# Optimization experiments

Hardware: AMD Instinct MI355X
Metric: run time of the kernel (lower is better)

The kernel has to match this reference:

```python
import jax, jax.numpy as jnp
import numpy as np

# Dimensions
NT, NS = 1000, 2048   # timesteps, basins
NF, NG = 6, 32        # forcing channels, static attributes
NH, NR, HS = 16, 8, 256  # buckets, routing taps, hidden size
NK, NGD = 3, 9        # len(kDict)=3 (km,ki,ke), len(gDict)=9


def setup_inputs() -> dict:
    key = jax.random.key(0)
    ks = jax.random.split(key, 16)
    # Physically plausible forcings: Prcp/Evp nonnegative, T1<=T2 (min/max temp)
    Prcp = jax.random.uniform(ks[0], (NT, NS)) * 10.0
    Evp = jax.random.uniform(ks[1], (NT, NS)) * 5.0
    Tm = jax.random.normal(ks[2], (NT, NS)) * 10.0
    T1 = Tm - jax.random.uniform(ks[3], (NT, NS)) * 5.0
    T2 = Tm + jax.random.uniform(ks[4], (NT, NS)) * 5.0
    Rad = jax.random.uniform(ks[5], (NT, NS))
    Hum = jax.random.uniform(ks[6], (NT, NS))
    x = jnp.stack([Prcp, Evp, T1, T2, Rad, Hum], axis=-1)  # [nt, ns, 6]
    xc = jax.random.normal(ks[7], (NS, NG))

    def lin(k, fan_in, fan_out, s=0.05):
        k1, k2 = jax.random.split(k)
        return (jax.random.normal(k1, (fan_in, fan_out)) * s,
                jax.random.normal(k2, (fan_out,)) * s)

    W_fc, b_fc = lin(ks[8], NG, HS)
    W_r, b_r = lin(ks[9], HS, NH * (NR + 1))
    W_g, b_g = lin(ks[10], HS, NH * NGD)
    W_kin, b_kin = lin(ks[11], 4, HS)
    W_kout, b_kout = lin(ks[12], HS, NH * NK)
    return dict(x=x, xc=xc, W_fc=W_fc, b_fc=b_fc, W_r=W_r, b_r=b_r,
                W_g=W_g, b_g=b_g, W_kin=W_kin, b_kin=b_kin,
                W_kout=W_kout, b_kout=b_kout)


def _hardsigmoid(v):
    return jnp.clip(v / 6.0 + 0.5, 0.0, 1.0)


def _forward(x, xc, W_fc, b_fc, W_r, b_r, W_g, b_g, W_kin, b_kin, W_kout, b_kout):
    nt, ns, _ = x.shape
    Prcp, Evp, T1, T2 = x[..., 0], x[..., 1], x[..., 2], x[..., 3]
    f = x[..., 2:]                        # [nt, ns, 4] (T1,T2,Rad,Hum)

    # ---- getParam (eval mode: DropMask is identity) ----
    state = xc @ W_fc + b_fc              # [ns, hs]
    pK = jnp.tanh(f @ W_kin + b_kin + state) @ W_kout + b_kout  # [nt, ns, nh*3]
    hG = jnp.tanh(state)
    pG = hG @ W_g + b_g                   # [ns, nh*9]
    pR = hG @ W_r + b_r                   # [ns, nh*(nr+1)]

    # sepParam(K): km=exp, ki=relu, ke=exp  -> time-varying [nt, ns, nh]
    km = jnp.exp(pK[..., 0 * NH:1 * NH])
    ki = jax.nn.relu(pK[..., 1 * NH:2 * NH])
    ke = jnp.exp(pK[..., 2 * NH:3 * NH])

    # sepParam(G): static [ns, nh]
    g = lambda i: pG[..., i * NH:(i + 1) * NH]
    kp = jax.nn.sigmoid(g(0))
    ks_ = jax.nn.sigmoid(g(1))
    kd = jax.nn.sigmoid(g(2))
    gd = jax.nn.sigmoid(g(3))
    gl = (jax.nn.sigmoid(g(4)) * 10.0) ** 3
    qb = jax.nn.relu(g(5)) / 10.0
    ga = jax.nn.softmax(g(6), axis=-1)    # area weights over buckets
    gi = _hardsigmoid(g(7)) / 2.0
    ge = jax.nn.relu(g(8))

    # onePeakWeight: unimodal routing weights [ns, nh, nr]
    r = pR.reshape(ns, NH, NR + 1)
    s = jax.nn.softmax(r, axis=-1)
    c = jnp.cumsum(s, axis=-1)
    w = jnp.minimum(c, 1.0 - c + s)[..., :NR]
    wr = w / jnp.sum(w, axis=-1, keepdims=True)

    # divideP: snow/liquid split from min/max temperature crossing 0 C
    fl = jnp.clip(T2 / (T2 - T1 + 1e-5), 0.0, 1.0)  # liquid fraction
    Pl = (Prcp * fl)[..., None]           # [nt, ns, 1]
    Ps = (Prcp * (1.0 - fl))[..., None]
    Ev = Evp[..., None]

    # ---- bucket.step recurrence over time (the custom-scan hot loop) ----
    def step(carry, inp):
        Sf, Ss, Sg = carry                # each [ns, nh]
        Ps_t, Pl_t, Ev_t, km_t, ki_t, ke_t = inp
        # snow bucket: accumulate, melt capped by degree-day factor km
        Sf = Sf + Ps_t
        qf = jnp.minimum(Sf, km_t)
        Sf = Sf - qf
        # partition inflow: impervious/direct fraction gi
        inflow = qf + Pl_t
        qd = inflow * gi
        Ss = Ss + inflow * (1.0 - gi)
        # evapotranspiration
        E = jnp.minimum(jnp.maximum(Ss, 0.0), Ev_t * ke_t * ge)
        Ss = Ss - E
        # interflow capped by ki
        qi = jnp.minimum(ki_t, jnp.maximum(Ss, 0.0))
        Ss = Ss - qi
        # quick flow above capacity gl, slow drainage below
        qp = kp * jnp.maximum(Ss - gl, 0.0)
        qsa = ks_ * jnp.clip(Ss, 0.0, gl)
        Ss = Ss - qp - qsa
        # deep/groundwater bucket: fraction gd percolates, linear reservoir kd + baseflow qb
        Sg = Sg + qsa * gd
        qg = kd * Sg + qb
        Sg = Sg * (1.0 - kd)
        q = qp + qsa * (1.0 - gd) + qg + qd + qi
        return (Sf, Ss, Sg), q

    init = (jnp.zeros((ns, NH), x.dtype),
            jnp.zeros((ns, NH), x.dtype),
            jnp.zeros((ns, NH), x.dtype))
    _, Qp = jax.lax.scan(step, init, (Ps, Pl, Ev, km, ki, ke))  # [nt, ns, nh]

    # routing: valid temporal convolution with per-bucket unit hydrograph wr
    Tout = nt - NR + 1
    Q = jnp.zeros((Tout, ns, NH), Qp.dtype)
    for rr in range(NR):  # NR is a small fixed constant
        Q = Q + Qp[NR - 1 - rr: nt - rr] * wr[..., rr]
    yOut = jnp.sum(Q * ga, axis=-1)       # [Tout, ns]
    return yOut


def reference(x, xc, W_fc, b_fc, W_r, b_r, W_g, b_g, W_kin, b_kin, W_kout, b_kout):
    return _forward(x, xc, W_fc, b_fc, W_r, b_r, W_g, b_g, W_kin, b_kin, W_kout, b_kout)
```

## Files before the change

kernel.cpp:

```cpp
#include <hip/hip_runtime.h>
#include <hip/hip_bf16.h>

#define NT   1000
#define NS   2048
#define NH   16
#define NR   8
#define HS   256
#define TOUT 993

typedef __attribute__((ext_vector_type(8))) short short8;
typedef __attribute__((ext_vector_type(4))) float f32x4;

__device__ __forceinline__ ushort f2bf(float f) {
    union { float f; unsigned int u; } v; v.f = f;
    unsigned int u = v.u;
    return (ushort)((u + 0x7fffu + ((u >> 16) & 1u)) >> 16);
}
__device__ __forceinline__ float bf2f(ushort u) {
    union { unsigned int i; float f; } v; v.i = ((unsigned int)u) << 16; return v.f;
}
__device__ __forceinline__ unsigned int packbf2(float lo, float hi) {
    union { __hip_bfloat162 b; unsigned int u; } v;
    v.b = __float22bfloat162_rn(make_float2(lo, hi));
    return v.u;
}
__device__ __forceinline__ float sigf(float x) { return 1.f / (1.f + __expf(-x)); }
__device__ __forceinline__ float fast_tanh(float z) {
    float e = exp2f(z * 2.885390082f);
    return 1.f - 2.f * __builtin_amdgcn_rcpf(e + 1.f);
}
template<int CTRL>
__device__ __forceinline__ float dpp_add(float v) {
    int s = __builtin_amdgcn_update_dpp(0, __builtin_bit_cast(int, v), CTRL, 0xf, 0xf, true);
    return v + __builtin_bit_cast(float, s);
}
__device__ __forceinline__ void gll16(const void* g, void* l) {
    __builtin_amdgcn_global_load_lds((const __attribute__((address_space(1))) unsigned int*)g,
                                     (__attribute__((address_space(3))) unsigned int*)l, 16, 0, 0);
}
__device__ __forceinline__ void gll4(const void* g, void* l) {
    __builtin_amdgcn_global_load_lds((const __attribute__((address_space(1))) unsigned int*)g,
                                     (__attribute__((address_space(3))) unsigned int*)l, 4, 0, 0);
}

__global__ __launch_bounds__(256) void kA(
    const float* __restrict__ xc, const float* __restrict__ W_fc, const float* __restrict__ b_fc,
    const float* __restrict__ W_r, const float* __restrict__ b_r,
    const float* __restrict__ W_g, const float* __restrict__ b_g,
    const float* __restrict__ W_kin, const float* __restrict__ b_kin,
    const float* __restrict__ W_kout,
    float* __restrict__ stateK, float* __restrict__ params,
    ushort* __restrict__ Wt_g, ushort* __restrict__ whlo_g)
{
    __shared__ float xcs[32];
    __shared__ float hG[256];
    __shared__ float pGR[288];
    const int s = blockIdx.x, tid = threadIdx.x;

    if (tid < 32) xcs[tid] = xc[s * 32 + tid];
    __syncthreads();

    float acc = b_fc[tid];
#pragma unroll 8
    for (int k = 0; k < 32; ++k) acc = fmaf(xcs[k], W_fc[k * 256 + tid], acc);
    stateK[s * 256 + tid] = acc + b_kin[tid];
    hG[tid] = tanhf(acc);
    __syncthreads();

    for (int j = tid; j < 288; j += 256) {
        const float* W = (j < 144) ? W_g : W_r;
        const float* b = (j < 144) ? b_g : b_r;
        int col = (j < 144) ? j : (j - 144);
        float a = b[col];
#pragma unroll 4
        for (int k = 0; k < 256; ++k) a = fmaf(hG[k], W[k * 144 + col], a);
        pGR[j] = a;
    }
    __syncthreads();

    if (tid < 16) {
        const int h = tid;
        float g0 = pGR[h],       g1 = pGR[16 + h],  g2 = pGR[32 + h];
        float g3 = pGR[48 + h],  g4 = pGR[64 + h],  g5 = pGR[80 + h];
        float g6 = pGR[96 + h],  g7 = pGR[112 + h], g8 = pGR[128 + h];
        float kp = sigf(g0), ksg = sigf(g1), kd = sigf(g2), gd = sigf(g3);
        float t4 = sigf(g4) * 10.f; float gl = t4 * t4 * t4;
        float qb = fmaxf(g5, 0.f) * 0.1f;
        float gi = fminf(fmaxf(g7 * (1.f / 6.f) + 0.5f, 0.f), 1.f) * 0.5f;
        float ge = fmaxf(g8, 0.f);
        float m = g6;
        for (int o = 1; o < 16; o <<= 1) m = fmaxf(m, __shfl_xor(m, o));
        float e = __expf(g6 - m), esum = e;
        for (int o = 1; o < 16; o <<= 1) esum += __shfl_xor(esum, o);
        float ga = e / esum;
        float r[9], rm = -1e30f;
#pragma unroll
        for (int i = 0; i < 9; ++i) { r[i] = pGR[144 + h * 9 + i]; rm = fmaxf(rm, r[i]); }
        float er[9], es = 0.f;
#pragma unroll
        for (int i = 0; i < 9; ++i) { er[i] = __expf(r[i] - rm); es += er[i]; }
        float inv_es = 1.f / es, c = 0.f, wsum = 0.f, w[8];
#pragma unroll
        for (int i = 0; i < 8; ++i) {
            float si = er[i] * inv_es; c += si;
            float wi = fminf(c, 1.f - c + si);
            w[i] = wi; wsum += wi;
        }
        const int base = s * 16 + h;
        params[0 * 32768 + base] = kp;       params[1 * 32768 + base] = ksg;
        params[2 * 32768 + base] = kd;       params[3 * 32768 + base] = gd;
        params[4 * 32768 + base] = gl;       params[5 * 32768 + base] = qb;
        params[6 * 32768 + base] = gi;       params[7 * 32768 + base] = 1.f - gi;
        params[8 * 32768 + base] = 1.f - kd; params[9 * 32768 + base] = 1.f - gd;
        params[10 * 32768 + base] = ge;
        float sc = ga / wsum;
#pragma unroll
        for (int i = 0; i < 8; ++i) params[(11 + i) * 32768 + base] = w[i] * sc;
    }

    if (s == 0) {
        for (int i = tid; i < 48 * 256; i += 256) {
            int col = i % 48, slot = i / 48;
            int kk = slot >> 5, q = (slot >> 3) & 3, j = slot & 7;
            int h = kk * 32 + ((j < 4) ? (q * 4 + j) : (16 + q * 4 + (j - 4)));
            Wt_g[col * 264 + slot] = f2bf(W_kout[h * 48 + col]);
        }
        {
            const int h = tid;
#pragma unroll
            for (int f = 0; f < 4; ++f) {
                float w = W_kin[f * 256 + h];
                ushort hi = f2bf(w);
                float lo = w - bf2f(hi);
                whlo_g[h * 8 + f] = hi;
                whlo_g[h * 8 + 4 + f] = f2bf(lo);
            }
        }
    }
}

__global__ __launch_bounds__(256, 3) void kB(
    const float* __restrict__ x,
    const float* __restrict__ stateK, const float* __restrict__ b_kout,
    const ushort* __restrict__ Wt_g, const ushort* __restrict__ whlo_g,
    const float* __restrict__ params,
    unsigned int* __restrict__ kmki, ushort* __restrict__ kevA,
    float2* __restrict__ pspl)
{
    __shared__ ushort Wt[48 * 264];
    __shared__ float  stS[16 * 260];
    __shared__ ushort whloS[2048];
    __shared__ float  geS[256];
    __shared__ float  evS[4][5][16];
    const int tid = threadIdx.x;
    const int st = blockIdx.x & 127;
    const int tg = blockIdx.x >> 7;
    const int s0 = st << 4;

    for (int i = tid; i < 3168; i += 256)
        ((uint2*)Wt)[i] = ((const uint2*)Wt_g)[i];
#pragma unroll
    for (int i = tid; i < 1024; i += 256) {
        int row = i >> 6, c = (i & 63) << 2;
        *(float4*)(stS + row * 260 + c) = *(const float4*)(stateK + (s0 + row) * 256 + c);
    }
    *(float4*)(whloS + tid * 8) = ((const float4*)whlo_g)[tid];
    geS[tid] = params[10 * 32768 + s0 * 16 + tid];
    __syncthreads();

    const int wv = tid >> 6, lane = tid & 63;
    const int mi = lane & 15, quad = lane >> 4;
    const int site = s0 + mi;
    const int t0 = tg * 20 + wv * 5;

    float xf[5][4];
#pragma unroll
    for (int ti = 0; ti < 5; ++ti) {
        const int t = t0 + ti;
        const int xb = (t * 2048 + site) * 6;
        float2 u23 = *(const float2*)(x + xb + 2);
        float2 u45 = *(const float2*)(x + xb + 4);
        xf[ti][0] = u23.x; xf[ti][1] = u23.y; xf[ti][2] = u45.x; xf[ti][3] = u45.y;
        if (lane < 16) {
            float2 u01 = *(const float2*)(x + xb);
            float fl = fminf(fmaxf(u23.y * __builtin_amdgcn_rcpf(u23.y - u23.x + 1e-5f), 0.f), 1.f);
            const int sg = st * 4 + (mi >> 2), sl = mi & 3;
            pspl[(sg * 1000 + t) * 4 + sl] = make_float2(u01.x * (1.f - fl), u01.x * fl);
            evS[wv][ti][mi] = u01.y;
        }
    }

    unsigned int bfr[5][4];
#pragma unroll
    for (int ti = 0; ti < 5; ++ti) {
        const float x0 = xf[ti][0], x1 = xf[ti][1], x2 = xf[ti][2], x3 = xf[ti][3];
        unsigned int h01 = packbf2(x0, x1), h23 = packbf2(x2, x3);
        float l0 = x0 - bf2f((ushort)(h01 & 0xffffu));
        float l1 = x1 - bf2f((ushort)(h01 >> 16));
        float l2 = x2 - bf2f((ushort)(h23 & 0xffffu));
        float l3 = x3 - bf2f((ushort)(h23 >> 16));
        unsigned int l01 = packbf2(l0, l1), l23 = packbf2(l2, l3);
        bfr[ti][0] = (quad == 0) ? h01 : (quad == 1 ? l01 : 0u);
        bfr[ti][1] = (quad == 0) ? h23 : (quad == 1 ? l23 : 0u);
        bfr[ti][2] = (quad == 0) ? h01 : 0u;
        bfr[ti][3] = (quad == 0) ? h23 : 0u;
    }

    const float*  stp = stS + mi * 260;
    const ushort* Wt0 = Wt + mi * 264 + quad * 8;
    const int q4 = quad * 4;

    f32x4 acc[5][3];
#pragma unroll
    for (int ti = 0; ti < 5; ++ti)
#pragma unroll
        for (int j = 0; j < 3; ++j) acc[ti][j] = (f32x4){0.f, 0.f, 0.f, 0.f};

#pragma unroll 1
    for (int kk = 0; kk < 8; ++kk) {
        const int ko = kk * 32;
        union { short8 s; unsigned int u[4]; } W0, W1, A0, A1;
        W0.s = *(const short8*)(whloS + (ko + mi) * 8);
        W1.s = *(const short8*)(whloS + (ko + 16 + mi) * 8);
        A0.u[0] = (quad <= 1) ? W0.u[0] : 0u;
        A0.u[1] = (quad <= 1) ? W0.u[1] : 0u;
        A0.u[2] = (quad == 0) ? W0.u[2] : 0u;
        A0.u[3] = (quad == 0) ? W0.u[3] : 0u;
        A1.u[0] = (quad <= 1) ? W1.u[0] : 0u;
        A1.u[1] = (quad <= 1) ? W1.u[1] : 0u;
        A1.u[2] = (quad == 0) ? W1.u[2] : 0u;
        A1.u[3] = (quad == 0) ? W1.u[3] : 0u;
        f32x4 c0 = *(const f32x4*)(stp + ko + q4);
        f32x4 c1 = *(const f32x4*)(stp + ko + 16 + q4);
        short8 b0 = *(const short8*)(Wt0 + ko);
        short8 b1 = *(const short8*)(Wt0 + 16 * 264 + ko);
        short8 b2 = *(const short8*)(Wt0 + 32 * 264 + ko);
#pragma unroll
        for (int ti = 0; ti < 5; ++ti) {
            union { short8 s; unsigned int u[4]; } B;
            B.u[0] = bfr[ti][0]; B.u[1] = bfr[ti][1];
            B.u[2] = bfr[ti][2]; B.u[3] = bfr[ti][3];
            f32x4 z0 = __builtin_amdgcn_mfma_f32_16x16x32_bf16(A0.s, B.s, c0, 0, 0, 0);
            f32x4 z1 = __builtin_amdgcn_mfma_f32_16x16x32_bf16(A1.s, B.s, c1, 0, 0, 0);
            union { short8 s; unsigned int u[4]; } a;
            a.u[0] = packbf2(fast_tanh(z0[0]), fast_tanh(z0[1]));
            a.u[1] = packbf2(fast_tanh(z0[2]), fast_tanh(z0[3]));
            a.u[2] = packbf2(fast_tanh(z1[0]), fast_tanh(z1[1]));
            a.u[3] = packbf2(fast_tanh(z1[2]), fast_tanh(z1[3]));
            acc[ti][0] = __builtin_amdgcn_mfma_f32_16x16x32_bf16(a.s, b0, acc[ti][0], 0, 0, 0);
            acc[ti][1] = __builtin_amdgcn_mfma_f32_16x16x32_bf16(a.s, b1, acc[ti][1], 0, 0, 0);
            acc[ti][2] = __builtin_amdgcn_mfma_f32_16x16x32_bf16(a.s, b2, acc[ti][2], 0, 0, 0);
        }
    }

    const float bo0 = b_kout[mi], bo1 = b_kout[16 + mi], bo2 = b_kout[32 + mi];
#pragma unroll
    for (int ti = 0; ti < 5; ++ti) {
        const int t = t0 + ti;
#pragma unroll
        for (int reg = 0; reg < 4; ++reg) {
            const int sl = quad * 4 + reg;
            float km = __expf(acc[ti][0][reg] + bo0);
            float ki = fmaxf(acc[ti][1][reg] + bo1, 0.f);
            float ke = __expf(acc[ti][2][reg] + bo2);
            float kev = ke * evS[wv][ti][sl] * geS[sl * 16 + mi];
            const int idx = ((s0 + sl) * 1000 + t) * 16 + mi;
            kmki[idx] = (unsigned int)f2bf(km) | ((unsigned int)f2bf(ki) << 16);
            kevA[idx] = f2bf(kev);
        }
    }
}

#define KM_STRIDE 4160
#define KE_BASE   16640
#define KE_STRIDE 2080
#define PS_BASE   24960
#define BUF_SZ    27008
__global__ __launch_bounds__(64, 1) void kC(
    const unsigned int* __restrict__ kmki, const ushort* __restrict__ kevA,
    const float2* __restrict__ pspl,
    const float* __restrict__ params, float* __restrict__ yOut)
{
    __shared__ char lds[2 * BUF_SZ];
    const int tid = threadIdx.x;
    const int sg = blockIdx.x;
    const int sl = tid >> 4;
    const int s = sg * 4 + sl;
    const int h = tid & 15;
    const int gid = s * 16 + h;

    const float kp  = params[0 * 32768 + gid];
    const float ks_ = params[1 * 32768 + gid];
    const float kd  = params[2 * 32768 + gid];
    const float gd  = params[3 * 32768 + gid];
    const float gl  = params[4 * 32768 + gid];
    const float qbv = params[5 * 32768 + gid];
    const float gi  = params[6 * 32768 + gid];
    const float gi1 = params[7 * 32768 + gid];
    const float kd1 = params[8 * 32768 + gid];
    const float gd1 = params[9 * 32768 + gid];
    float wrga[8];
#pragma unroll
    for (int i = 0; i < 8; ++i) wrga[i] = params[(11 + i) * 32768 + gid];

    float Sf = 0.f, Ss = 0.f, Sg = 0.f;
    float qh[8];
#pragma unroll
    for (int i = 0; i < 8; ++i) qh[i] = 0.f;

    const char* kmG = (const char*)kmki;
    const char* keG = (const char*)kevA;
    const char* psG = (const char*)pspl;

#define STAGE(c, TAIL) do {                                                     \
        char* L = lds + ((c) & 1) * BUF_SZ;                                     \
        _Pragma("unroll")                                                       \
        for (int q = 0; q < 4; ++q) {                                           \
            const char* gk = kmG + ((size_t)(sg * 4 + q) * 1000 + (c) * 64) * 64; \
            const char* ge = keG + ((size_t)(sg * 4 + q) * 1000 + (c) * 64) * 32; \
            char* lk = L + q * KM_STRIDE;                                       \
            char* le = L + KE_BASE + q * KE_STRIDE;                             \
            if (!(TAIL)) {                                                      \
                _Pragma("unroll")                                               \
                for (int k = 0; k < 4; ++k) gll16(gk + k * 1024 + tid * 16, lk + k * 1024); \
                _Pragma("unroll")                                               \
                for (int k = 0; k < 2; ++k) gll16(ge + k * 1024 + tid * 16, le + k * 1024); \
            } else {                                                            \
                _Pragma("unroll")                                               \
                for (int k = 0; k < 2; ++k) gll16(gk + k * 1024 + tid * 16, lk + k * 1024); \
                _Pragma("unroll")                                               \
                for (int k = 0; k < 2; ++k) gll4(gk + 2048 + k * 256 + tid * 4, lk + 2048 + k * 256); \
                gll16(ge + tid * 16, le);                                       \
                gll4(ge + 1024 + tid * 4, le + 1024);                           \
            }                                                                   \
        }                                                                       \
        const char* gp = psG + ((size_t)sg * 1000 + (c) * 64) * 32;             \
        char* lp = L + PS_BASE;                                                 \
        if (!(TAIL)) { gll16(gp + tid * 16, lp); gll16(gp + 1024 + tid * 16, lp + 1024); } \
        else         { gll16(gp + tid * 16, lp); gll4(gp + 1024 + tid * 4, lp + 1024); }   \
    } while (0)

#define COMPUTE(c, NSB) do {                                                    \
        const char* L = lds + ((c) & 1) * BUF_SZ;                               \
        const char* lk = L + sl * KM_STRIDE + h * 4;                            \
        const char* le = L + KE_BASE + sl * KE_STRIDE + h * 2;                  \
        const char* lp = L + PS_BASE + sl * 8;                                  \
        for (int sb = 0; sb < (NSB); ++sb) {                                    \
            unsigned int a[8]; ushort e[8]; float2 p[8];                        \
            _Pragma("unroll")                                                   \
            for (int i = 0; i < 8; ++i) {                                       \
                const int tt = sb * 8 + i;                                      \
                a[i] = *(const unsigned int*)(lk + tt * 64);                    \
                e[i] = *(const ushort*)(le + tt * 32);                          \
                p[i] = *(const float2*)(lp + tt * 32);                          \
            }                                                                   \
            float z[8];                                                         \
            _Pragma("unroll")                                                   \
            for (int i = 0; i < 8; ++i) {                                       \
                float km = __builtin_bit_cast(float, a[i] << 16);               \
                float ki = __builtin_bit_cast(float, a[i] & 0xffff0000u);       \
                float kev = __builtin_bit_cast(float, ((unsigned int)e[i]) << 16); \
                float ps = p[i].x, pl = p[i].y;                                 \
                Sf += ps;                                                       \
                float qf = fminf(Sf, km); Sf -= qf;                             \
                float inflow = qf + pl;                                         \
                float qd = inflow * gi;                                         \
                Ss = fmaf(inflow, gi1, Ss);                                     \
                float E = fminf(Ss, kev); Ss -= E;                              \
                float qi = fminf(ki, Ss); Ss -= qi;                             \
                float qp = kp * fmaxf(Ss - gl, 0.f);                            \
                float qsa = ks_ * fminf(Ss, gl);                                \
                Ss -= qp + qsa;                                                 \
                Sg = fmaf(qsa, gd, Sg);                                         \
                float qg = fmaf(kd, Sg, qbv);                                   \
                Sg *= kd1;                                                      \
                float q = fmaf(qsa, gd1, qp) + qg + qd + qi;                    \
                qh[i] = q;                                                      \
                float v = 0.f;                                                  \
                _Pragma("unroll")                                               \
                for (int k = 0; k < 8; ++k) v = fmaf(wrga[k], qh[(i - k) & 7], v); \
                z[i] = v;                                                       \
            }                                                                   \
            _Pragma("unroll")                                                   \
            for (int i = 0; i < 8; ++i) z[i] = dpp_add<0xB1>(z[i]);             \
            _Pragma("unroll")                                                   \
            for (int i = 0; i < 8; ++i) z[i] = dpp_add<0x4E>(z[i]);             \
            _Pragma("unroll")                                                   \
            for (int i = 0; i < 8; ++i) z[i] = dpp_add<0x141>(z[i]);            \
            _Pragma("unroll")                                                   \
            for (int i = 0; i < 8; ++i) z[i] = dpp_add<0x140>(z[i]);            \
            if (h == 0) {                                                       \
                _Pragma("unroll")                                               \
                for (int i = 0; i < 8; ++i) {                                   \
                    const int t = (c) * 64 + sb * 8 + i;                        \
                    if (t >= 7) yOut[(t - 7) * 2048 + s] = z[i];                \
                }                                                               \
            }                                                                   \
        }                                                                       \
    } while (0)

    STAGE(0, false);
    for (int c = 0; c < 16; ++c) {
        if (c < 15) {
            if (c + 1 == 15) STAGE(15, true);
            else             STAGE(c + 1, false);
            asm volatile("s_waitcnt vmcnt(26)" ::: "memory");
        } else {
            asm volatile("s_waitcnt vmcnt(0)" ::: "memory");
        }
        if (c == 15) COMPUTE(15, 5);
        else         COMPUTE(c, 8);
        asm volatile("" ::: "memory");
    }
#undef STAGE
#undef COMPUTE
}

extern "C" void kernel_launch(void* const* d_in, const int* in_sizes, int n_in,
                              void* d_out, int out_size, void* d_ws, size_t ws_size,
                              hipStream_t stream) {
    const float* x      = (const float*)d_in[0];
    const float* xc     = (const float*)d_in[1];
    const float* W_fc   = (const float*)d_in[2];
    const float* b_fc   = (const float*)d_in[3];
    const float* W_r    = (const float*)d_in[4];
    const float* b_r    = (const float*)d_in[5];
    const float* W_g    = (const float*)d_in[6];
    const float* b_g    = (const float*)d_in[7];
    const float* W_kin  = (const float*)d_in[8];
    const float* b_kin  = (const float*)d_in[9];
    const float* W_kout = (const float*)d_in[10];
    const float* b_kout = (const float*)d_in[11];
    float* yOut = (float*)d_out;

    char* ws = (char*)d_ws;
    float*  stateK = (float*)(ws + 0);
    float*  params = (float*)(ws + (2 << 20));
    ushort* Wt_g   = (ushort*)(ws + (6 << 20));
    ushort* whlo_g = (ushort*)(ws + (6 << 20) + (64 << 10));
    char*   p      = ws + (6 << 20) + (128 << 10);
    float2* pspl   = (float2*)p;
    unsigned int* kmki = (unsigned int*)(p + 16384000);
    ushort* kevA   = (ushort*)(p + 16384000 + 131072000);

    hipLaunchKernelGGL(kA, dim3(2048), dim3(256), 0, stream,
                       xc, W_fc, b_fc, W_r, b_r, W_g, b_g, W_kin, b_kin, W_kout,
                       stateK, params, Wt_g, whlo_g);
    hipLaunchKernelGGL(kB, dim3(128 * 50), dim3(256), 0, stream,
                       x, stateK, b_kout, Wt_g, whlo_g, params, kmki, kevA, pspl);
    hipLaunchKernelGGL(kC, dim3(512), dim3(64), 0, stream,
                       kmki, kevA, pspl, params, yOut);
}
```

Measured before the change: 528.3 us.

## Software-pipeline routing convolution one block behind the bucket scan

Splits the per-8-step block into a scan phase and a convolution/reduce/store phase. The convolution for the previous block runs after the current block's scan, so the serial scan dependency chain can interleave with independent FMA, DPP and store work. The convolution also uses two partial accumulators to shorten its own chain. This costs extra registers for the two history arrays, adds a trailing flush call, and forces the loops not to unroll.

```diff
diff --git a/kernel.cpp b/kernel.cpp
--- a/kernel.cpp
+++ b/kernel.cpp
@@ -304,9 +304,9 @@
     for (int i = 0; i < 8; ++i) wrga[i] = params[(11 + i) * 32768 + gid];
 
     float Sf = 0.f, Ss = 0.f, Sg = 0.f;
-    float qh[8];
-#pragma unroll
-    for (int i = 0; i < 8; ++i) qh[i] = 0.f;
+    float qcur[8], qp1[8], qp2[8];
+#pragma unroll
+    for (int i = 0; i < 8; ++i) { qcur[i] = 0.f; qp1[i] = 0.f; qp2[i] = 0.f; }
 
     const char* kmG = (const char*)kmki;
     const char* keG = (const char*)kevA;
@@ -340,66 +340,75 @@
         else         { gll16(gp + tid * 16, lp); gll4(gp + 1024 + tid * 4, lp + 1024); }   \
     } while (0)
 
-#define COMPUTE(c, NSB) do {                                                    \
+#define SCANB(c, sb) do {                                                       \
         const char* L = lds + ((c) & 1) * BUF_SZ;                               \
-        const char* lk = L + sl * KM_STRIDE + h * 4;                            \
-        const char* le = L + KE_BASE + sl * KE_STRIDE + h * 2;                  \
-        const char* lp = L + PS_BASE + sl * 8;                                  \
-        for (int sb = 0; sb < (NSB); ++sb) {                                    \
-            unsigned int a[8]; ushort e[8]; float2 p[8];                        \
+        const char* lk = L + sl * KM_STRIDE + h * 4 + (sb) * 512;               \
+        const char* le = L + KE_BASE + sl * KE_STRIDE + h * 2 + (sb) * 256;     \
+        const char* lp = L + PS_BASE + sl * 8 + (sb) * 256;                     \
+        unsigned int a[8]; ushort e[8]; float2 p[8];                            \
+        _Pragma("unroll")                                                       \
+        for (int i = 0; i < 8; ++i) {                                           \
+            a[i] = *(const unsigned int*)(lk + i * 64);                         \
+            e[i] = *(const ushort*)(le + i * 32);                               \
+            p[i] = *(const float2*)(lp + i * 32);                               \
+        }                                                                       \
+        _Pragma("unroll")                                                       \
+        for (int i = 0; i < 8; ++i) {                                           \
+            float km = __builtin_bit_cast(float, a[i] << 16);                   \
+            float ki = __builtin_bit_cast(float, a[i] & 0xffff0000u);           \
+            float kev = __builtin_bit_cast(float, ((unsigned int)e[i]) << 16);  \
+            float ps = p[i].x, pl = p[i].y;                                     \
+            Sf += ps;                                                           \
+            float qf = fminf(Sf, km); Sf -= qf;                                 \
+            float inflow = qf + pl;                                             \
+            float qd = inflow * gi;                                             \
+            Ss = fmaf(inflow, gi1, Ss);                                         \
+            float E = fminf(Ss, kev); Ss -= E;                                  \
+            float qi = fminf(ki, Ss); Ss -= qi;                                 \
+            float qp = kp * fmaxf(Ss - gl, 0.f);                                \
+            float qsa = ks_ * fminf(Ss, gl);                                    \
+            Ss -= qp + qsa;                                                     \
+            Sg = fmaf(qsa, gd, Sg);                                             \
+            float qg = fmaf(kd, Sg, qbv);                                       \
+            Sg *= kd1;                                                          \
+            qcur[i] = fmaf(qsa, gd1, qp) + qg + qd + qi;                        \
+        }                                                                       \
+    } while (0)
+
+#define CONV_STORE(m) do {                                                      \
+        float z[8];                                                             \
+        _Pragma("unroll")                                                       \
+        for (int i = 0; i < 8; ++i) {                                           \
+            float za = wrga[6] * ((i >= 6) ? qp1[i - 6] : qp2[i + 2]);          \
+            za = fmaf(wrga[4], (i >= 4) ? qp1[i - 4] : qp2[i + 4], za);         \
+            za = fmaf(wrga[2], (i >= 2) ? qp1[i - 2] : qp2[i + 6], za);         \
+            za = fmaf(wrga[0], qp1[i], za);                                     \
+            float zb = wrga[7] * ((i >= 7) ? qp1[i - 7] : qp2[i + 1]);          \
+            zb = fmaf(wrga[5], (i >= 5) ? qp1[i - 5] : qp2[i + 3], zb);         \
+            zb = fmaf(wrga[3], (i >= 3) ? qp1[i - 3] : qp2[i + 5], zb);         \
+            zb = fmaf(wrga[1], (i >= 1) ? qp1[i - 1] : qp2[i + 7], zb);         \
+            z[i] = za + zb;                                                     \
+        }                                                                       \
+        _Pragma("unroll")                                                       \
+        for (int i = 0; i < 8; ++i) z[i] = dpp_add<0xB1>(z[i]);                 \
+        _Pragma("unroll")                                                       \
+        for (int i = 0; i < 8; ++i) z[i] = dpp_add<0x4E>(z[i]);                 \
+        _Pragma("unroll")                                                       \
+        for (int i = 0; i < 8; ++i) z[i] = dpp_add<0x141>(z[i]);                \
+        _Pragma("unroll")                                                       \
+        for (int i = 0; i < 8; ++i) z[i] = dpp_add<0x140>(z[i]);                \
+        if (h == 0) {                                                           \
             _Pragma("unroll")                                                   \
             for (int i = 0; i < 8; ++i) {                                       \
-                const int tt = sb * 8 + i;                                      \
-                a[i] = *(const unsigned int*)(lk + tt * 64);                    \
-                e[i] = *(const ushort*)(le + tt * 32);                          \
-                p[i] = *(const float2*)(lp + tt * 32);                          \
-            }                                                                   \
-            float z[8];                                                         \
-            _Pragma("unroll")                                                   \
-            for (int i = 0; i < 8; ++i) {                                       \
-                float km = __builtin_bit_cast(float, a[i] << 16);               \
-                float ki = __builtin_bit_cast(float, a[i] & 0xffff0000u);       \
-                float kev = __builtin_bit_cast(float, ((unsigned int)e[i]) << 16); \
-                float ps = p[i].x, pl = p[i].y;                                 \
-                Sf += ps;                                                       \
-                float qf = fminf(Sf, km); Sf -= qf;                             \
-                float inflow = qf + pl;                                         \
-                float qd = inflow * gi;                                         \
-                Ss = fmaf(inflow, gi1, Ss);                                     \
-                float E = fminf(Ss, kev); Ss -= E;                              \
-                float qi = fminf(ki, Ss); Ss -= qi;                             \
-                float qp = kp * fmaxf(Ss - gl, 0.f);                            \
-                float qsa = ks_ * fminf(Ss, gl);                                \
-                Ss -= qp + qsa;                                                 \
-                Sg = fmaf(qsa, gd, Sg);                                         \
-                float qg = fmaf(kd, Sg, qbv);                                   \
-                Sg *= kd1;                                                      \
-                float q = fmaf(qsa, gd1, qp) + qg + qd + qi;                    \
-                qh[i] = q;                                                      \
-                float v = 0.f;                                                  \
-                _Pragma("unroll")                                               \
-                for (int k = 0; k < 8; ++k) v = fmaf(wrga[k], qh[(i - k) & 7], v); \
-                z[i] = v;                                                       \
-            }                                                                   \
-            _Pragma("unroll")                                                   \
-            for (int i = 0; i < 8; ++i) z[i] = dpp_add<0xB1>(z[i]);             \
-            _Pragma("unroll")                                                   \
-            for (int i = 0; i < 8; ++i) z[i] = dpp_add<0x4E>(z[i]);             \
-            _Pragma("unroll")                                                   \
-            for (int i = 0; i < 8; ++i) z[i] = dpp_add<0x141>(z[i]);            \
-            _Pragma("unroll")                                                   \
-            for (int i = 0; i < 8; ++i) z[i] = dpp_add<0x140>(z[i]);            \
-            if (h == 0) {                                                       \
-                _Pragma("unroll")                                               \
-                for (int i = 0; i < 8; ++i) {                                   \
-                    const int t = (c) * 64 + sb * 8 + i;                        \
-                    if (t >= 7) yOut[(t - 7) * 2048 + s] = z[i];                \
-                }                                                               \
+                const int t = (m) * 8 + i;                                      \
+                if (t >= 7) yOut[(t - 7) * 2048 + s] = z[i];                    \
             }                                                                   \
         }                                                                       \
     } while (0)
 
     STAGE(0, false);
+    int g = 0;
+#pragma unroll 1
     for (int c = 0; c < 16; ++c) {
         if (c < 15) {
             if (c + 1 == 15) STAGE(15, true);
@@ -408,12 +417,20 @@
         } else {
             asm volatile("s_waitcnt vmcnt(0)" ::: "memory");
         }
-        if (c == 15) COMPUTE(15, 5);
-        else         COMPUTE(c, 8);
+        const int NSB = (c == 15) ? 5 : 8;
+#pragma unroll 1
+        for (int sb = 0; sb < NSB; ++sb, ++g) {
+            SCANB(c, sb);
+            CONV_STORE(g - 1);
+#pragma unroll
+            for (int i = 0; i < 8; ++i) { qp2[i] = qp1[i]; qp1[i] = qcur[i]; }
+        }
         asm volatile("" ::: "memory");
     }
+    CONV_STORE(124);
 #undef STAGE
-#undef COMPUTE
+#undef SCANB
+#undef CONV_STORE
 }
 
 extern "C" void kernel_launch(void* const* d_in, const int* in_sizes, int n_in,
```

After: 519.3 us. No clear change (-1.7%).
